# Kernel optimization log

Hardware: AMD Instinct MI355X
Metric: run time of the kernel (lower is better)

Reference implementation:

```python
import jax, jax.numpy as jnp
import numpy as np

N, IN_F, OUT_F, HEADS = 4096, 512, 128, 8
ALPHA = 0.2
MASK_VAL = -9e15


def setup_inputs() -> dict:
    key = jax.random.key(0)
    k1, k2, k3, k4 = jax.random.split(key, 4)
    node_features = jax.random.normal(k1, (N, IN_F), dtype=jnp.float32)
    adj_matrix = jax.random.randint(k2, (N, N), 0, 2).astype(jnp.int32)
    # xavier_uniform-style scales
    w_lim = 1.414 * np.sqrt(6.0 / (IN_F + HEADS * OUT_F))
    a_lim = 1.414 * np.sqrt(6.0 / (2 * OUT_F + HEADS))
    W = jax.random.uniform(k3, (IN_F, HEADS * OUT_F), jnp.float32, -w_lim, w_lim)
    a = jax.random.uniform(k4, (2 * OUT_F, HEADS), jnp.float32, -a_lim, a_lim)
    return {"node_features": node_features, "adj_matrix": adj_matrix, "W": W, "a": a}


def reference(node_features, adj_matrix, W, a):
    n = node_features.shape[0]
    # (N, H, F) per-head projected features
    h = (node_features @ W).reshape(n, HEADS, OUT_F)
    # decompose e[i,j,h] = a_l . h_i + a_r . h_j (exactly equals the cat/matmul form)
    a_l, a_r = a[:OUT_F], a[OUT_F:]                      # (F, H) each
    left = jnp.einsum('nhf,fh->nh', h, a_l)              # (N, H)
    right = jnp.einsum('nhf,fh->nh', h, a_r)             # (N, H)
    e = left[:, None, :] + right[None, :, :]             # (N, N, H)
    e = jnp.where(e > 0, e, ALPHA * e)                   # LeakyReLU(alpha)
    e = jnp.where(adj_matrix[:, :, None] > 0, e, MASK_VAL)
    attn = jax.nn.softmax(e, axis=1)                     # softmax over source nodes j
    # dropout skipped (eval mode / rate 0.0)
    out = jnp.einsum('ijh,jhf->ihf', attn, h).reshape(n, HEADS * OUT_F)
    return jax.nn.elu(out)
```

## Files before the change

### kernel.cpp

```cpp
#include <hip/hip_runtime.h>
#include <stdint.h>

#define NN 4096
#define KIN 512
#define NH 8
#define DF 128
#define HID 1024

typedef __attribute__((ext_vector_type(8))) short bf16x8;
typedef __attribute__((ext_vector_type(4))) float f32x4;
typedef __attribute__((ext_vector_type(8))) unsigned short u16x8;
typedef __attribute__((ext_vector_type(4))) unsigned int u32x4;
typedef unsigned short u16;
typedef unsigned long long u64;

__device__ __forceinline__ u16 f2bf(float x){
  unsigned int u = __float_as_uint(x);
  return (u16)((u + 0x7fffu + ((u >> 16) & 1u)) >> 16);
}

__device__ __forceinline__ float fexp2(float x){
#if __has_builtin(__builtin_amdgcn_exp2f)
  return __builtin_amdgcn_exp2f(x);
#else
  return exp2f(x);
#endif
}

__device__ __forceinline__ void gload16(const void* g, void* lds){
  __builtin_amdgcn_global_load_lds(
      (const __attribute__((address_space(1))) unsigned int*)g,
      (__attribute__((address_space(3))) unsigned int*)lds, 16, 0, 0);
}

__global__ __launch_bounds__(256) void k_pack(const int4* __restrict__ adj,
                                              unsigned char* __restrict__ bm){
  int idx = blockIdx.x * 256 + threadIdx.x;
  int4 a = adj[idx * 2];
  int4 b = adj[idx * 2 + 1];
  unsigned int m = (a.x != 0)        | ((a.y != 0) << 1) | ((a.z != 0) << 2) |
                   ((a.w != 0) << 3) | ((b.x != 0) << 4) | ((b.y != 0) << 5) |
                   ((b.z != 0) << 6) | ((b.w != 0) << 7);
  bm[idx] = (unsigned char)m;
}

__global__ __launch_bounds__(256) void k_conv(const float* __restrict__ X,
                                              const float* __restrict__ W,
                                              u16* __restrict__ A2,
                                              u16* __restrict__ WT){
  int idx = blockIdx.x * 256 + threadIdx.x;
  if (idx < NN * KIN) A2[idx] = f2bf(X[idx]);
  if (idx < HID * KIN){
    int n = idx / KIN, k = idx % KIN;
    WT[idx] = f2bf(W[k * HID + n]);
  }
}

__global__ __launch_bounds__(256) void k_gemm(const u16* __restrict__ A2,
                                              const u16* __restrict__ BT,
                                              float* __restrict__ C){
  __shared__ u16 As[8192], Bs[8192];
  const int tid = threadIdx.x;
  const int l = tid & 63, w = tid >> 6;
  const int wr = w >> 1, wc = w & 1;
  const int ib = blockIdx.x >> 3, nb = blockIdx.x & 7;
  const int p = l >> 4;
  f32x4 acc[4][4] = {};
  for (int k0 = 0; k0 < KIN; k0 += 64){
    __syncthreads();
    #pragma unroll
    for (int q = 0; q < 4; q++){
      int beta = ((q << 8) + tid) << 4;
      int row = beta >> 7, inner = beta & 127;
      int gin = inner ^ ((row & 7) << 4);
      gload16(A2 + (size_t)(ib * 128 + row) * KIN + k0 + (gin >> 1), (char*)As + beta);
      gload16(BT + (size_t)(nb * 128 + row) * KIN + k0 + (gin >> 1), (char*)Bs + beta);
    }
    __syncthreads();
    #pragma unroll
    for (int kk = 0; kk < 2; kk++){
      bf16x8 af[4], bfv[4];
      const int kb = ((kk << 5) + (p << 3)) << 1;
      #pragma unroll
      for (int m = 0; m < 4; m++){
        int r = wr * 64 + m * 16 + (l & 15);
        af[m] = *(const bf16x8*)((const char*)As + r * 128 + (kb ^ ((r & 7) << 4)));
      }
      #pragma unroll
      for (int n = 0; n < 4; n++){
        int r = wc * 64 + n * 16 + (l & 15);
        bfv[n] = *(const bf16x8*)((const char*)Bs + r * 128 + (kb ^ ((r & 7) << 4)));
      }
      #pragma unroll
      for (int m = 0; m < 4; m++)
        #pragma unroll
        for (int n = 0; n < 4; n++)
          acc[m][n] = __builtin_amdgcn_mfma_f32_16x16x32_bf16(af[m], bfv[n], acc[m][n], 0, 0, 0);
    }
  }
  #pragma unroll
  for (int m = 0; m < 4; m++)
    #pragma unroll
    for (int n = 0; n < 4; n++)
      #pragma unroll
      for (int r4 = 0; r4 < 4; r4++){
        int row = ib * 128 + wr * 64 + m * 16 + p * 4 + r4;
        int col = nb * 128 + wc * 64 + n * 16 + (l & 15);
        C[(size_t)row * HID + col] = acc[m][n][r4];
      }
}

__global__ __launch_bounds__(256) void k_lr(const float* __restrict__ h,
                                            const float* __restrict__ a,
                                            float* __restrict__ Lg,
                                            float* __restrict__ Rg){
  const int i = blockIdx.x;
  const int t = threadIdx.x;
  const int hd = t >> 5, l32 = t & 31;
  const int f = l32 << 2;
  const float4 hv = *(const float4*)(h + (size_t)i * HID + hd * DF + f);
  float pl = hv.x * a[(f + 0) * NH + hd] + hv.y * a[(f + 1) * NH + hd]
           + hv.z * a[(f + 2) * NH + hd] + hv.w * a[(f + 3) * NH + hd];
  float pr = hv.x * a[(128 + f + 0) * NH + hd] + hv.y * a[(128 + f + 1) * NH + hd]
           + hv.z * a[(128 + f + 2) * NH + hd] + hv.w * a[(128 + f + 3) * NH + hd];
  #pragma unroll
  for (int s = 1; s < 32; s <<= 1){
    pl += __shfl_xor(pl, s);
    pr += __shfl_xor(pr, s);
  }
  if (l32 == 0){
    int idx = hd * NN + i;
    Lg[idx] = pl * 1.44269504089f;
    Rg[idx] = pr * 1.44269504089f;
  }
}

__global__ __launch_bounds__(256) void k_tr(const float* __restrict__ h,
                                            u16* __restrict__ HT){
  __shared__ u16 T[64][80];
  const int it = blockIdx.x & 63, ft = blockIdx.x >> 6;
  const int i0 = it * 64, f0 = ft * 64;
  const int t = threadIdx.x;
  const int r = t >> 4, c = (t & 15) << 2;
  #pragma unroll
  for (int q = 0; q < 4; q++){
    int row = r + q * 16;
    float4 v = *(const float4*)(h + (size_t)(i0 + row) * HID + f0 + c);
    T[c + 0][row] = f2bf(v.x);
    T[c + 1][row] = f2bf(v.y);
    T[c + 2][row] = f2bf(v.z);
    T[c + 3][row] = f2bf(v.w);
  }
  __syncthreads();
  const int fr = t >> 2, c0 = (t & 3) << 4;
  u16x8 v0 = *(const u16x8*)&T[fr][c0];
  u16x8 v1 = *(const u16x8*)&T[fr][c0 + 8];
  *(u16x8*)(HT + (size_t)(f0 + fr) * NN + i0 + c0)     = v0;
  *(u16x8*)(HT + (size_t)(f0 + fr) * NN + i0 + c0 + 8) = v1;
}

template<int JSPLIT>
__global__ __launch_bounds__(256) void k_agg(const u16* __restrict__ HT,
                                             const unsigned char* __restrict__ bm,
                                             const float* __restrict__ Lg,
                                             const float* __restrict__ Rg,
                                             float* __restrict__ P0,
                                             float* __restrict__ P1,
                                             float* __restrict__ P2,
                                             float* __restrict__ P3,
                                             float* __restrict__ Dbase){
  __shared__ u16 Hs[2 * 8192];
  const int b = blockIdx.x;
  const int hd = b & 7;
  const int ib = (b >> 3) & 63;
  const int jq = b >> 9;
  const int i0 = ib * 64;
  const int jbase = jq * (NN / JSPLIT);
  const int NT = (NN / JSPLIT) >> 6;
  const int tid = threadIdx.x;
  const int w = tid >> 6, l = tid & 63;
  const int p = l >> 4;
  const int row_l = (w << 4) + (l & 15);
  const int gi = i0 + row_l;
  const float lgv = Lg[hd * NN + gi];
  const float* Rr = Rg + hd * NN;
  const u64* bmrow = (const u64*)(bm + (size_t)gi * 512);
  const u16* src = HT + (size_t)hd * DF * NN;
  f32x4 acc[8] = {};
  f32x4 accd = {};
  const short one_bf = (short)0x3F80;
  const bf16x8 ones = {one_bf, one_bf, one_bf, one_bf, one_bf, one_bf, one_bf, one_bf};

  auto stage = [&](int d, int j0s){
    #pragma unroll
    for (int q = 0; q < 4; q++){
      int beta = ((q << 8) + tid) << 4;
      int fr = beta >> 7, inner = beta & 127;
      int gin = inner ^ ((fr & 7) << 4);
      gload16(src + (size_t)fr * NN + j0s + (gin >> 1), (char*)Hs + d * 16384 + beta);
    }
  };

  stage(0, jbase);
  __syncthreads();

  for (int jt = 0; jt < NT; ++jt){
    const int j0 = jbase + (jt << 6);
    const int cur = jt & 1;
    if (jt < NT - 1) stage(cur ^ 1, j0 + 64);

    const u64 bmv = bmrow[j0 >> 6];

    bf16x8 af[2];
    #pragma unroll
    for (int kk = 0; kk < 2; kk++){
      const int jb = j0 + (kk << 5) + (p << 3);
      const float4 rv0 = *(const float4*)(Rr + jb);
      const float4 rv1 = *(const float4*)(Rr + jb + 4);
      const unsigned int bbits = (unsigned int)(bmv >> (((kk << 2) + p) << 3)) & 0xffu;
      const float r8[8] = {rv0.x, rv0.y, rv0.z, rv0.w, rv1.x, rv1.y, rv1.z, rv1.w};
      float w8[8];
      #pragma unroll
      for (int e = 0; e < 8; e++){
        float s = lgv + r8[e];
        float t = fmaxf(s, 0.2f * s);
        t = ((bbits >> e) & 1u) ? t : -131072.f;
        w8[e] = fexp2(t);
      }
      unsigned int q0, q1, q2, q3;
      asm volatile("v_cvt_pk_bf16_f32 %0, %1, %2" : "=v"(q0) : "v"(w8[0]), "v"(w8[1]));
      asm volatile("v_cvt_pk_bf16_f32 %0, %1, %2" : "=v"(q1) : "v"(w8[2]), "v"(w8[3]));
      asm volatile("v_cvt_pk_bf16_f32 %0, %1, %2" : "=v"(q2) : "v"(w8[4]), "v"(w8[5]));
      asm volatile("v_cvt_pk_bf16_f32 %0, %1, %2" : "=v"(q3) : "v"(w8[6]), "v"(w8[7]));
      u32x4 uu = {q0, q1, q2, q3};
      af[kk] = __builtin_bit_cast(bf16x8, uu);
      accd = __builtin_amdgcn_mfma_f32_16x16x32_bf16(af[kk], ones, accd, 0, 0, 0);
    }

    const char* hb = (const char*)Hs + cur * 16384;
    #pragma unroll
    for (int kk = 0; kk < 2; kk++){
      const int kb = ((kk << 5) + (p << 3)) << 1;
      #pragma unroll
      for (int n = 0; n < 8; n++){
        const int fr = (n << 4) + (l & 15);
        bf16x8 bfr = *(const bf16x8*)(hb + fr * 128 + (kb ^ ((fr & 7) << 4)));
        acc[n] = __builtin_amdgcn_mfma_f32_16x16x32_bf16(af[kk], bfr, acc[n], 0, 0, 0);
      }
    }
    __syncthreads();
  }

  float* P = (jq == 0) ? P0 : (jq == 1) ? P1 : (jq == 2) ? P2 : P3;
  float* D = Dbase + jq * NH * NN;
  if ((l & 15) == 0){
    #pragma unroll
    for (int r4 = 0; r4 < 4; r4++)
      D[hd * NN + i0 + (w << 4) + (p << 2) + r4] = accd[r4];
  }

  const int rowbase = i0 + (w << 4) + (p << 2);
  #pragma unroll
  for (int r4 = 0; r4 < 4; r4++){
    const int grow = rowbase + r4;
    float* orow = P + (size_t)grow * HID + hd * DF;
    #pragma unroll
    for (int n = 0; n < 8; n++)
      orow[(n << 4) + (l & 15)] = acc[n][r4];
  }
}

template<int JS>
__global__ __launch_bounds__(256) void k_comb(const float* __restrict__ P1,
                                              const float* __restrict__ P2,
                                              const float* __restrict__ P3,
                                              const float* __restrict__ Db,
                                              float* __restrict__ out){
  const int idx = blockIdx.x * 256 + threadIdx.x;
  const int i  = idx >> 8;
  const int c4 = idx & 255;
  const int hd = c4 >> 5;
  float d = Db[hd * NN + i] + Db[NH * NN + hd * NN + i];
  if (JS == 4) d += Db[2 * NH * NN + hd * NN + i] + Db[3 * NH * NN + hd * NN + i];
  const float rinv = 1.0f / d;
  float4 a0 = ((const float4*)out)[idx];
  float4 a1 = ((const float4*)P1)[idx];
  float4 v;
  v.x = a0.x + a1.x; v.y = a0.y + a1.y; v.z = a0.z + a1.z; v.w = a0.w + a1.w;
  if (JS == 4){
    float4 a2 = ((const float4*)P2)[idx];
    float4 a3 = ((const float4*)P3)[idx];
    v.x += a2.x + a3.x; v.y += a2.y + a3.y; v.z += a2.z + a3.z; v.w += a2.w + a3.w;
  }
  v.x *= rinv; v.y *= rinv; v.z *= rinv; v.w *= rinv;
  v.x = v.x > 0.f ? v.x : (expf(v.x) - 1.0f);
  v.y = v.y > 0.f ? v.y : (expf(v.y) - 1.0f);
  v.z = v.z > 0.f ? v.z : (expf(v.z) - 1.0f);
  v.w = v.w > 0.f ? v.w : (expf(v.w) - 1.0f);
  ((float4*)out)[idx] = v;
}

extern "C" void kernel_launch(void* const* d_in, const int* in_sizes, int n_in,
                              void* d_out, int out_size, void* d_ws, size_t ws_size,
                              hipStream_t stream) {
  const float* X   = (const float*)d_in[0];
  const int*   adj = (const int*)d_in[1];
  const float* W   = (const float*)d_in[2];
  const float* a   = (const float*)d_in[3];
  float* out = (float*)d_out;

  char* ws = (char*)d_ws;
  size_t off = 0;
  float* h  = (float*)(ws + off);        off += (size_t)NN * HID * 4;
  u16*   A2 = (u16*)(ws + off);          off += (size_t)NN * KIN * 2;
  u16*   WT = (u16*)(ws + off);          off += (size_t)HID * KIN * 2;
  u16*   HT = (u16*)(ws + off);          off += (size_t)HID * NN * 2;
  unsigned char* bmp = (unsigned char*)(ws + off); off += (size_t)NN * 512;
  float* Lg = (float*)(ws + off);        off += (size_t)NH * NN * 4;
  float* Rg = (float*)(ws + off);        off += (size_t)NH * NN * 4;
  float* P2 = (float*)(ws + off);
  float* P3 = P2 + (size_t)NN * HID;
  const size_t need4 = off + 2 * (size_t)NN * HID * 4;

  float* P0 = out;
  float* P1 = h;
  float* Db = (float*)A2;

  const bool quarters = ws_size >= need4;

  k_pack<<<dim3(NN * NN / 8 / 256), dim3(256), 0, stream>>>((const int4*)adj, bmp);
  k_conv<<<dim3(NN * KIN / 256), dim3(256), 0, stream>>>(X, W, A2, WT);
  k_gemm<<<dim3(256), dim3(256), 0, stream>>>(A2, WT, h);
  k_lr  <<<dim3(NN), dim3(256), 0, stream>>>(h, a, Lg, Rg);
  k_tr  <<<dim3(1024), dim3(256), 0, stream>>>(h, HT);
  if (quarters){
    k_agg<4><<<dim3(2048), dim3(256), 0, stream>>>(HT, bmp, Lg, Rg, P0, P1, P2, P3, Db);
    k_comb<4><<<dim3(NN * HID / 1024), dim3(256), 0, stream>>>(P1, P2, P3, Db, out);
  } else {
    k_agg<2><<<dim3(1024), dim3(256), 0, stream>>>(HT, bmp, Lg, Rg, P0, P1, P2, P3, Db);
    k_comb<2><<<dim3(NN * HID / 1024), dim3(256), 0, stream>>>(P1, P2, P3, Db, out);
  }
}
```

Baseline: 146.0 us.

## Process two 16-row fragments per wave to reuse staged H tiles

Doubles the row tile of the aggregation kernel from 64 to 128 rows, with each wave computing two 16-row attention-weight fragments that share the same LDS B-fragment loads. This halves HT staging traffic and the R-vector loads per row and halves the grid size. It costs more accumulator registers per thread, which may reduce occupancy, and gives fewer blocks per CU.

```diff
diff --git a/kernel.cpp b/kernel.cpp
--- a/kernel.cpp
+++ b/kernel.cpp
@@ -172,22 +172,24 @@
   __shared__ u16 Hs[2 * 8192];
   const int b = blockIdx.x;
   const int hd = b & 7;
-  const int ib = (b >> 3) & 63;
-  const int jq = b >> 9;
-  const int i0 = ib * 64;
+  const int ib = (b >> 3) & 31;
+  const int jq = b >> 8;
+  const int i0 = ib * 128;
   const int jbase = jq * (NN / JSPLIT);
   const int NT = (NN / JSPLIT) >> 6;
   const int tid = threadIdx.x;
   const int w = tid >> 6, l = tid & 63;
   const int p = l >> 4;
-  const int row_l = (w << 4) + (l & 15);
-  const int gi = i0 + row_l;
-  const float lgv = Lg[hd * NN + gi];
+  const int gi0 = i0 + w * 32 + (l & 15);
+  const int gi1 = gi0 + 16;
+  const float lg0 = Lg[hd * NN + gi0];
+  const float lg1 = Lg[hd * NN + gi1];
   const float* Rr = Rg + hd * NN;
-  const u64* bmrow = (const u64*)(bm + (size_t)gi * 512);
+  const u64* bmrow0 = (const u64*)(bm + (size_t)gi0 * 512);
+  const u64* bmrow1 = (const u64*)(bm + (size_t)gi1 * 512);
   const u16* src = HT + (size_t)hd * DF * NN;
-  f32x4 acc[8] = {};
-  f32x4 accd = {};
+  f32x4 acc0[8] = {}, acc1[8] = {};
+  f32x4 accd0 = {}, accd1 = {};
   const short one_bf = (short)0x3F80;
   const bf16x8 ones = {one_bf, one_bf, one_bf, one_bf, one_bf, one_bf, one_bf, one_bf};
 
@@ -209,32 +211,55 @@
     const int cur = jt & 1;
     if (jt < NT - 1) stage(cur ^ 1, j0 + 64);
 
-    const u64 bmv = bmrow[j0 >> 6];
-
-    bf16x8 af[2];
+    const u64 bmv0 = bmrow0[j0 >> 6];
+    const u64 bmv1 = bmrow1[j0 >> 6];
+
+    bf16x8 af0[2], af1[2];
     #pragma unroll
     for (int kk = 0; kk < 2; kk++){
       const int jb = j0 + (kk << 5) + (p << 3);
       const float4 rv0 = *(const float4*)(Rr + jb);
       const float4 rv1 = *(const float4*)(Rr + jb + 4);
-      const unsigned int bbits = (unsigned int)(bmv >> (((kk << 2) + p) << 3)) & 0xffu;
       const float r8[8] = {rv0.x, rv0.y, rv0.z, rv0.w, rv1.x, rv1.y, rv1.z, rv1.w};
-      float w8[8];
-      #pragma unroll
-      for (int e = 0; e < 8; e++){
-        float s = lgv + r8[e];
-        float t = fmaxf(s, 0.2f * s);
-        t = ((bbits >> e) & 1u) ? t : -131072.f;
-        w8[e] = fexp2(t);
-      }
-      unsigned int q0, q1, q2, q3;
-      asm volatile("v_cvt_pk_bf16_f32 %0, %1, %2" : "=v"(q0) : "v"(w8[0]), "v"(w8[1]));
-      asm volatile("v_cvt_pk_bf16_f32 %0, %1, %2" : "=v"(q1) : "v"(w8[2]), "v"(w8[3]));
-      asm volatile("v_cvt_pk_bf16_f32 %0, %1, %2" : "=v"(q2) : "v"(w8[4]), "v"(w8[5]));
-      asm volatile("v_cvt_pk_bf16_f32 %0, %1, %2" : "=v"(q3) : "v"(w8[6]), "v"(w8[7]));
-      u32x4 uu = {q0, q1, q2, q3};
-      af[kk] = __builtin_bit_cast(bf16x8, uu);
-      accd = __builtin_amdgcn_mfma_f32_16x16x32_bf16(af[kk], ones, accd, 0, 0, 0);
+      const unsigned int sh = (unsigned int)(((kk << 2) + p) << 3);
+      const unsigned int bb0 = (unsigned int)(bmv0 >> sh) & 0xffu;
+      const unsigned int bb1 = (unsigned int)(bmv1 >> sh) & 0xffu;
+      {
+        float w8[8];
+        #pragma unroll
+        for (int e = 0; e < 8; e++){
+          float s = lg0 + r8[e];
+          float t = fmaxf(s, 0.2f * s);
+          t = ((bb0 >> e) & 1u) ? t : -131072.f;
+          w8[e] = fexp2(t);
+        }
+        unsigned int q0, q1, q2, q3;
+        asm volatile("v_cvt_pk_bf16_f32 %0, %1, %2" : "=v"(q0) : "v"(w8[0]), "v"(w8[1]));
+        asm volatile("v_cvt_pk_bf16_f32 %0, %1, %2" : "=v"(q1) : "v"(w8[2]), "v"(w8[3]));
+        asm volatile("v_cvt_pk_bf16_f32 %0, %1, %2" : "=v"(q2) : "v"(w8[4]), "v"(w8[5]));
+        asm volatile("v_cvt_pk_bf16_f32 %0, %1, %2" : "=v"(q3) : "v"(w8[6]), "v"(w8[7]));
+        u32x4 uu = {q0, q1, q2, q3};
+        af0[kk] = __builtin_bit_cast(bf16x8, uu);
+        accd0 = __builtin_amdgcn_mfma_f32_16x16x32_bf16(af0[kk], ones, accd0, 0, 0, 0);
+      }
+      {
+        float w8[8];
+        #pragma unroll
+        for (int e = 0; e < 8; e++){
+          float s = lg1 + r8[e];
+          float t = fmaxf(s, 0.2f * s);
+          t = ((bb1 >> e) & 1u) ? t : -131072.f;
+          w8[e] = fexp2(t);
+        }
+        unsigned int q0, q1, q2, q3;
+        asm volatile("v_cvt_pk_bf16_f32 %0, %1, %2" : "=v"(q0) : "v"(w8[0]), "v"(w8[1]));
+        asm volatile("v_cvt_pk_bf16_f32 %0, %1, %2" : "=v"(q1) : "v"(w8[2]), "v"(w8[3]));
+        asm volatile("v_cvt_pk_bf16_f32 %0, %1, %2" : "=v"(q2) : "v"(w8[4]), "v"(w8[5]));
+        asm volatile("v_cvt_pk_bf16_f32 %0, %1, %2" : "=v"(q3) : "v"(w8[6]), "v"(w8[7]));
+        u32x4 uu = {q0, q1, q2, q3};
+        af1[kk] = __builtin_bit_cast(bf16x8, uu);
+        accd1 = __builtin_amdgcn_mfma_f32_16x16x32_bf16(af1[kk], ones, accd1, 0, 0, 0);
+      }
     }
 
     const char* hb = (const char*)Hs + cur * 16384;
@@ -245,7 +270,8 @@
       for (int n = 0; n < 8; n++){
         const int fr = (n << 4) + (l & 15);
         bf16x8 bfr = *(const bf16x8*)(hb + fr * 128 + (kb ^ ((fr & 7) << 4)));
-        acc[n] = __builtin_amdgcn_mfma_f32_16x16x32_bf16(af[kk], bfr, acc[n], 0, 0, 0);
+        acc0[n] = __builtin_amdgcn_mfma_f32_16x16x32_bf16(af0[kk], bfr, acc0[n], 0, 0, 0);
+        acc1[n] = __builtin_amdgcn_mfma_f32_16x16x32_bf16(af1[kk], bfr, acc1[n], 0, 0, 0);
       }
     }
     __syncthreads();
@@ -255,18 +281,22 @@
   float* D = Dbase + jq * NH * NN;
   if ((l & 15) == 0){
     #pragma unroll
-    for (int r4 = 0; r4 < 4; r4++)
-      D[hd * NN + i0 + (w << 4) + (p << 2) + r4] = accd[r4];
-  }
-
-  const int rowbase = i0 + (w << 4) + (p << 2);
+    for (int r4 = 0; r4 < 4; r4++){
+      D[hd * NN + i0 + w * 32 + (p << 2) + r4]      = accd0[r4];
+      D[hd * NN + i0 + w * 32 + 16 + (p << 2) + r4] = accd1[r4];
+    }
+  }
+
+  const int rowbase = i0 + w * 32 + (p << 2);
   #pragma unroll
   for (int r4 = 0; r4 < 4; r4++){
-    const int grow = rowbase + r4;
-    float* orow = P + (size_t)grow * HID + hd * DF;
-    #pragma unroll
-    for (int n = 0; n < 8; n++)
-      orow[(n << 4) + (l & 15)] = acc[n][r4];
+    float* orow0 = P + (size_t)(rowbase + r4) * HID + hd * DF;
+    float* orow1 = P + (size_t)(rowbase + 16 + r4) * HID + hd * DF;
+    #pragma unroll
+    for (int n = 0; n < 8; n++){
+      orow0[(n << 4) + (l & 15)] = acc0[n][r4];
+      orow1[(n << 4) + (l & 15)] = acc1[n][r4];
+    }
   }
 }
 
@@ -334,10 +364,10 @@
   k_lr  <<<dim3(NN), dim3(256), 0, stream>>>(h, a, Lg, Rg);
   k_tr  <<<dim3(1024), dim3(256), 0, stream>>>(h, HT);
   if (quarters){
-    k_agg<4><<<dim3(2048), dim3(256), 0, stream>>>(HT, bmp, Lg, Rg, P0, P1, P2, P3, Db);
+    k_agg<4><<<dim3(1024), dim3(256), 0, stream>>>(HT, bmp, Lg, Rg, P0, P1, P2, P3, Db);
     k_comb<4><<<dim3(NN * HID / 1024), dim3(256), 0, stream>>>(P1, P2, P3, Db, out);
   } else {
-    k_agg<2><<<dim3(1024), dim3(256), 0, stream>>>(HT, bmp, Lg, Rg, P0, P1, P2, P3, Db);
+    k_agg<2><<<dim3(512), dim3(256), 0, stream>>>(HT, bmp, Lg, Rg, P0, P1, P2, P3, Db);
     k_comb<2><<<dim3(NN * HID / 1024), dim3(256), 0, stream>>>(P1, P2, P3, Db, out);
   }
 }
```

New measurement: 151.9 us. 4.0% more time.
